# Optimization experiments

Hardware: AMD Instinct MI355X
Metric: run time of the kernel (lower is better)

## Reference

```python
import jax, jax.numpy as jnp
import numpy as np

B, F, H = 16384, 2048, 4096   # batch, n_features, n_hidden
D, K = 4096, 2048             # num_of_demos, num_of_features


def setup_inputs() -> dict:
    key = jax.random.key(0)
    ks = jax.random.split(key, 16)
    s = 0.02
    return {
        "x": jax.random.normal(ks[0], (B, F), jnp.float32),
        "demo_metric": jax.random.uniform(ks[1], (D, K), jnp.float32),
        "alpha": jax.random.normal(ks[2], (K,), jnp.float32),
        "sample_loss": jax.random.uniform(ks[3], (D, K), jnp.float32),
        "subdom_constant": jax.random.uniform(ks[4], (1,), jnp.float32),
        "num_of_demos": D,
        "num_of_features": K,
        "W1": jax.random.normal(ks[5], (F, H), jnp.float32) * s,
        "b1": jnp.zeros((H,), jnp.float32),
        "W2": jax.random.normal(ks[6], (H, H), jnp.float32) * s,
        "b2": jnp.zeros((H,), jnp.float32),
        "W3": jax.random.normal(ks[7], (H, H), jnp.float32) * s,
        "b3": jnp.zeros((H,), jnp.float32),
        "W4": jax.random.normal(ks[8], (H, 2), jnp.float32) * s,
        "b4": jnp.zeros((2,), jnp.float32),
    }


def reference(x, demo_metric, alpha, sample_loss, subdom_constant,
              num_of_demos, num_of_features,
              W1, b1, W2, b2, W3, b3, W4, b4):
    # subdom hinge loss: max(alpha_k * (sample_loss_jk - demo_loss_jk) + 1, 0) - c
    margin = alpha[None, :] * (sample_loss - demo_metric) + 1.0  # [D, K]
    subdom = jnp.maximum(margin, 0.0) - subdom_constant          # broadcast c
    loss = jnp.sum(subdom)

    # MLP classifier (dropout = identity at inference) + sigmoid
    h = jax.nn.relu(x @ W1 + b1)
    h = jax.nn.relu(h @ W2 + b2)
    h = jax.nn.relu(h @ W3 + b3)
    probs = jax.nn.sigmoid(h @ W4 + b4)  # [B, 2]
    return (loss, probs)
```

## Files before the change

### kernel.cpp

```cpp
#include <hip/hip_runtime.h>
#include <cstdint>
#include <cstddef>

typedef unsigned short u16;
typedef __attribute__((ext_vector_type(8))) __bf16 bf16x8;
typedef __attribute__((ext_vector_type(4))) float f32x4;

__device__ __forceinline__ u16 f2bf(float f) {
  union { float f; unsigned u; } v; v.f = f;
  unsigned r = v.u + 0x7FFFu + ((v.u >> 16) & 1u);
  return (u16)(r >> 16);
}
__device__ __forceinline__ float bf2f(unsigned h) {
  union { unsigned u; float f; } v; v.u = h << 16;
  return v.f;
}

__global__ void init_loss_kernel(const float* __restrict__ c,
                                 const int* __restrict__ D,
                                 const int* __restrict__ K,
                                 float* __restrict__ out) {
  out[0] = -c[0] * (float)D[0] * (float)K[0];
}

__global__ void subdom_kernel(const float4* __restrict__ dm,
                              const float4* __restrict__ sl,
                              const float4* __restrict__ alpha4,
                              float* __restrict__ out, int n4, int k4mask) {
  const int stride = gridDim.x * blockDim.x;
  float s = 0.f;
  for (int i = blockIdx.x * blockDim.x + threadIdx.x; i < n4; i += stride) {
    float4 d = dm[i], l = sl[i], a = alpha4[i & k4mask];
    s += fmaxf(fmaf(a.x, l.x - d.x, 1.f), 0.f);
    s += fmaxf(fmaf(a.y, l.y - d.y, 1.f), 0.f);
    s += fmaxf(fmaf(a.z, l.z - d.z, 1.f), 0.f);
    s += fmaxf(fmaf(a.w, l.w - d.w, 1.f), 0.f);
  }
#pragma unroll
  for (int off = 32; off > 0; off >>= 1) s += __shfl_down(s, off, 64);
  __shared__ float red[4];
  const int lane = threadIdx.x & 63, wave = threadIdx.x >> 6;
  if (lane == 0) red[wave] = s;
  __syncthreads();
  if (threadIdx.x == 0) atomicAdd(out, red[0] + red[1] + red[2] + red[3]);
}

__global__ void cast_f32_bf16_kernel(const float4* __restrict__ in,
                                     u16* __restrict__ out, int n4) {
  const int stride = gridDim.x * blockDim.x;
  for (int i = blockIdx.x * blockDim.x + threadIdx.x; i < n4; i += stride) {
    float4 v = in[i];
    uint2 p;
    p.x = (unsigned)f2bf(v.x) | ((unsigned)f2bf(v.y) << 16);
    p.y = (unsigned)f2bf(v.z) | ((unsigned)f2bf(v.w) << 16);
    ((uint2*)out)[i] = p;
  }
}

__global__ void transpose_cast_kernel(const float* __restrict__ in,
                                      u16* __restrict__ out, int K, int N) {
  __shared__ float tile[32][33];
  const int bx = blockIdx.x * 32;
  const int by = blockIdx.y * 32;
  const int tx = threadIdx.x, ty = threadIdx.y;
#pragma unroll
  for (int i = ty; i < 32; i += 8)
    tile[i][tx] = in[(size_t)(by + i) * N + bx + tx];
  __syncthreads();
#pragma unroll
  for (int i = ty; i < 32; i += 8)
    out[(size_t)(bx + i) * K + by + tx] = f2bf(tile[tx][i]);
}


__device__ __forceinline__ void gload_lds16(const void* g, void* l) {
  __builtin_amdgcn_global_load_lds(
      (const __attribute__((address_space(1))) void*)g,
      (__attribute__((address_space(3))) void*)l, 16, 0, 0);
}

#define VMW(N) asm volatile("s_waitcnt vmcnt(" #N ")" ::: "memory")
#define MF(a, b, c) __builtin_amdgcn_mfma_f32_16x16x32_bf16(a, b, c, 0, 0, 0)

#define STAGE_A(BU, Q, TK)                                                    \
  gload_lds16(A + aGbase + (size_t)((Q)*64) * K + (size_t)(TK)*64,            \
              (void*)(As + ((BU)*4 + (Q)) * 4096 + swave))

#define STAGE_B(BU, NH, HH, TK)                                               \
  gload_lds16(Bt + bGbase + (size_t)((NH)*32 + (HH)*128) * K +                \
                  (size_t)(TK)*64,                                            \
              (void*)(Bs + ((BU)*2 + (NH)) * 8192 + (HH)*4096 + swave))

#define BRD(BF, BU, NH2)                                                      \
  {                                                                           \
    const u16* Br_ = Bs + ((BU)*2 + (NH2)) * 8192 + bbase;                    \
    BF[0] = *(const bf16x8*)(Br_ + aslot0);                                   \
    BF[1] = *(const bf16x8*)(Br_ + aslot1);                                   \
    BF[2] = *(const bf16x8*)(Br_ + 1024 + aslot0);                            \
    BF[3] = *(const bf16x8*)(Br_ + 1024 + aslot1);                            \
  }

#define PH(BUF, MH, NH, LA, BF, PRE_CODE, STAGE_CODE, WAIT_CODE)              \
  {                                                                           \
    if (LA) {                                                                 \
      const u16* Ar_ = As + ((BUF)*4 + (wm << 1) + (MH)) * 4096 + abase;      \
      _Pragma("unroll") for (int f_ = 0; f_ < 4; ++f_) {                      \
        af0[f_] = *(const bf16x8*)(Ar_ + f_ * 1024 + aslot0);                 \
        af1[f_] = *(const bf16x8*)(Ar_ + f_ * 1024 + aslot1);                 \
      }                                                                       \
    }                                                                         \
    PRE_CODE;                                                                 \
    STAGE_CODE;                                                               \
    __builtin_amdgcn_s_setprio(1);                                            \
    _Pragma("unroll") for (int f_ = 0; f_ < 4; ++f_) {                        \
      acc[(MH)*4 + f_][(NH)*2 + 0] = MF(af0[f_], BF[0], acc[(MH)*4 + f_][(NH)*2 + 0]); \
      acc[(MH)*4 + f_][(NH)*2 + 0] = MF(af1[f_], BF[1], acc[(MH)*4 + f_][(NH)*2 + 0]); \
      acc[(MH)*4 + f_][(NH)*2 + 1] = MF(af0[f_], BF[2], acc[(MH)*4 + f_][(NH)*2 + 1]); \
      acc[(MH)*4 + f_][(NH)*2 + 1] = MF(af1[f_], BF[3], acc[(MH)*4 + f_][(NH)*2 + 1]); \
    }                                                                         \
    __builtin_amdgcn_s_setprio(0);                                            \
    WAIT_CODE;                                                                \
    __builtin_amdgcn_s_barrier();                                             \
  }

__global__ __launch_bounds__(512, 2) void gemm256(
    const u16* __restrict__ A, const u16* __restrict__ Bt,
    const float* __restrict__ bias, u16* __restrict__ C,
    int M, int N, int K, int act) {
  __shared__ __align__(16) u16 As[2 * 4 * 4096];
  __shared__ __align__(16) u16 Bs[2 * 2 * 8192];

  const int gx = gridDim.x;
  const int bid = blockIdx.x + blockIdx.y * gx;
  const int cpx = (gx * gridDim.y) >> 3;
  const int tilei = (bid & 7) * cpx + (bid >> 3);
  const int m0 = (tilei / gx) * 256;
  const int n0 = (tilei % gx) * 256;

  const int tid = threadIdx.x;
  const int wave = tid >> 6, lane = tid & 63;
  const int l15 = lane & 15, quad = lane >> 4;
  const int wm = wave >> 2, wn = wave & 3;
  const int lsw = l15 & 7;

  const int aslot0 = ((quad ^ lsw) << 3);
  const int aslot1 = (((4 + quad) ^ lsw) << 3);
  const int abase = l15 * 64;
  const int bbase = (wn * 32 + l15) * 64;

  const int srow = tid >> 3;
  const int skch = ((tid & 7) ^ (srow & 7)) << 3;
  const int brow = ((srow >> 5) << 6) + (srow & 31);
  const size_t aGbase = (size_t)(m0 + srow) * K + skch;
  const size_t bGbase = (size_t)(n0 + brow) * K + skch;
  const int swave = wave * 512;

  f32x4 acc[8][4];
#pragma unroll
  for (int i = 0; i < 8; ++i)
#pragma unroll
    for (int j = 0; j < 4; ++j) acc[i][j] = (f32x4){0.f, 0.f, 0.f, 0.f};
  bf16x8 af0[4], af1[4], bfr0[4], bfr1[4];

  STAGE_A(0, 0, 0); STAGE_A(0, 1, 0); STAGE_A(0, 2, 0); STAGE_A(0, 3, 0);
  STAGE_B(0, 0, 0, 0); STAGE_B(0, 0, 1, 0);
  STAGE_B(0, 1, 0, 0); STAGE_B(0, 1, 1, 0);
  STAGE_A(1, 0, 1); STAGE_A(1, 2, 1);
  VMW(2);
  __builtin_amdgcn_s_barrier();
  BRD(bfr0, 0, 0);

  const int niter = K >> 7;
  for (int it = 0; it < niter - 1; ++it) {
    const int t1 = 2 * it + 1, t2 = 2 * it + 2, t3 = 2 * it + 3;
    PH(0, 0, 0, 1, bfr0, {},
       { STAGE_B(1, 0, 0, t1); STAGE_B(1, 0, 1, t1); }, { VMW(6); });
    PH(0, 0, 1, 0, bfr1, BRD(bfr1, 0, 1),
       { STAGE_B(1, 1, 0, t1); STAGE_B(1, 1, 1, t1); }, { VMW(4); });
    PH(0, 1, 0, 1, bfr0, {},
       { STAGE_A(0, 0, t2); STAGE_A(0, 2, t2); }, { VMW(4); });
    PH(0, 1, 1, 0, bfr1, BRD(bfr0, 1, 0),
       { STAGE_A(1, 1, t1); STAGE_A(1, 3, t1); }, {});
    PH(1, 0, 0, 1, bfr0, {},
       { STAGE_B(0, 0, 0, t2); STAGE_B(0, 0, 1, t2); }, { VMW(6); });
    PH(1, 0, 1, 0, bfr1, BRD(bfr1, 1, 1),
       { STAGE_B(0, 1, 0, t2); STAGE_B(0, 1, 1, t2); }, { VMW(4); });
    PH(1, 1, 0, 1, bfr0, {},
       { STAGE_A(1, 0, t3); STAGE_A(1, 2, t3); }, { VMW(4); });
    PH(1, 1, 1, 0, bfr1, BRD(bfr0, 0, 0),
       { STAGE_A(0, 1, t2); STAGE_A(0, 3, t2); }, {});
  }
  {
    const int t1 = 2 * niter - 1;
    PH(0, 0, 0, 1, bfr0, {},
       { STAGE_B(1, 0, 0, t1); STAGE_B(1, 0, 1, t1); }, { VMW(6); });
    PH(0, 0, 1, 0, bfr1, BRD(bfr1, 0, 1),
       { STAGE_B(1, 1, 0, t1); STAGE_B(1, 1, 1, t1); }, { VMW(4); });
    PH(0, 1, 0, 1, bfr0, {}, {}, { VMW(2); });
    PH(0, 1, 1, 0, bfr1, BRD(bfr0, 1, 0),
       { STAGE_A(1, 1, t1); STAGE_A(1, 3, t1); }, {});
    PH(1, 0, 0, 1, bfr0, {}, {}, { VMW(2); });
    PH(1, 0, 1, 0, bfr1, BRD(bfr1, 1, 1), {}, { VMW(0); });
    PH(1, 1, 0, 1, bfr0, {}, {}, {});
    PH(1, 1, 1, 0, bfr1, {}, {}, {});
  }

#pragma unroll
  for (int mi = 0; mi < 8; ++mi) {
    const int row = m0 + wm * 128 + (mi >> 2) * 64 + (mi & 3) * 16 + quad * 4;
#pragma unroll
    for (int j = 0; j < 4; ++j) {
      const int col = n0 + wn * 64 + j * 16 + l15;
      const float bv = bias[col];
#pragma unroll
      for (int r = 0; r < 4; ++r) {
        float v = acc[mi][j][r] + bv;
        if (act) v = fmaxf(v, 0.f);
        C[(size_t)(row + r) * N + col] = f2bf(v);
      }
    }
  }
}

__global__ __launch_bounds__(256) void head_kernel(
    const u16* __restrict__ h, const float2* __restrict__ W4,
    const float* __restrict__ b4, float* __restrict__ out, int H) {
  const int row = blockIdx.x;
  const u16* hr = h + (size_t)row * H;
  const int tid = threadIdx.x;
  float p0 = 0.f, p1 = 0.f;
#pragma unroll
  for (int ii = 0; ii < 2; ++ii) {
    const int base = tid * 16 + ii * 8;
    const uint4 hv = *(const uint4*)(hr + base);
    const unsigned uu[4] = {hv.x, hv.y, hv.z, hv.w};
#pragma unroll
    for (int j = 0; j < 4; ++j) {
      float a0 = bf2f(uu[j] & 0xffffu);
      float a1 = bf2f(uu[j] >> 16);
      float2 w0 = W4[base + 2 * j];
      float2 w1 = W4[base + 2 * j + 1];
      p0 += a0 * w0.x + a1 * w1.x;
      p1 += a0 * w0.y + a1 * w1.y;
    }
  }
#pragma unroll
  for (int off = 32; off > 0; off >>= 1) {
    p0 += __shfl_down(p0, off, 64);
    p1 += __shfl_down(p1, off, 64);
  }
  __shared__ float r0[4], r1[4];
  const int lane = tid & 63, wave = tid >> 6;
  if (lane == 0) { r0[wave] = p0; r1[wave] = p1; }
  __syncthreads();
  if (tid == 0) {
    float l0 = r0[0] + r0[1] + r0[2] + r0[3] + b4[0];
    float l1 = r1[0] + r1[1] + r1[2] + r1[3] + b4[1];
    out[1 + row * 2] = 1.f / (1.f + __expf(-l0));
    out[2 + row * 2] = 1.f / (1.f + __expf(-l1));
  }
}

extern "C" void kernel_launch(void* const* d_in, const int* in_sizes, int n_in,
                              void* d_out, int out_size, void* d_ws,
                              size_t ws_size, hipStream_t stream) {
  (void)in_sizes; (void)n_in; (void)out_size; (void)ws_size;
  const float* x  = (const float*)d_in[0];
  const float* dm = (const float*)d_in[1];
  const float* al = (const float*)d_in[2];
  const float* sl = (const float*)d_in[3];
  const float* sc = (const float*)d_in[4];
  const int*   nd = (const int*)d_in[5];
  const int*   nf = (const int*)d_in[6];
  const float* W1 = (const float*)d_in[7];
  const float* b1 = (const float*)d_in[8];
  const float* W2 = (const float*)d_in[9];
  const float* b2 = (const float*)d_in[10];
  const float* W3 = (const float*)d_in[11];
  const float* b3 = (const float*)d_in[12];
  const float* W4 = (const float*)d_in[13];
  const float* b4 = (const float*)d_in[14];
  float* out = (float*)d_out;

  const int B = 16384, F = 2048, H = 4096, D = 4096, K = 2048;

  char* ws = (char*)d_ws;
  u16* xb = (u16*)ws;
  u16* wt = (u16*)(ws + (size_t)B * F * 2);
  u16* hA = (u16*)(ws + (size_t)B * F * 2 + (size_t)H * H * 2);
  u16* hB = hA + (size_t)B * H;

  init_loss_kernel<<<1, 1, 0, stream>>>(sc, nd, nf, out);
  subdom_kernel<<<1024, 256, 0, stream>>>((const float4*)dm, (const float4*)sl,
                                          (const float4*)al, out, D * K / 4,
                                          K / 4 - 1);
  cast_f32_bf16_kernel<<<4096, 256, 0, stream>>>((const float4*)x, xb, B * F / 4);
  transpose_cast_kernel<<<dim3(H / 32, F / 32), dim3(32, 8), 0, stream>>>(W1, wt, F, H);
  gemm256<<<dim3(H / 256, B / 256), 512, 0, stream>>>(xb, wt, b1, hA, B, H, F, 1);
  transpose_cast_kernel<<<dim3(H / 32, H / 32), dim3(32, 8), 0, stream>>>(W2, wt, H, H);
  gemm256<<<dim3(H / 256, B / 256), 512, 0, stream>>>(hA, wt, b2, hB, B, H, H, 1);
  transpose_cast_kernel<<<dim3(H / 32, H / 32), dim3(32, 8), 0, stream>>>(W3, wt, H, H);
  gemm256<<<dim3(H / 256, B / 256), 512, 0, stream>>>(hB, wt, b3, hA, B, H, H, 1);
  head_kernel<<<B, 256, 0, stream>>>(hA, (const float2*)W4, b4, out, H);
}
```

Before: 1.691 ms.

## Restructure GEMM pipeline to prefetch LDS fragments after MFMA and batch global stages

Reorders the software pipeline of the 256x256 bf16 GEMM so that LDS reads of A and B fragments for the next phase are issued after the current MFMA block, behind a sched_barrier, instead of before it. Global-to-LDS staging is regrouped into two larger batches per half-iteration, with the prologue staging only one K-tile. The goal is to hide LDS read latency behind MFMA work and to simplify the wait-count schedule. The risks are higher register pressure from holding prefetched fragments across barriers, and less overlap of global loads because the prologue stages less ahead.

Result: slower. 1.879 ms (+11.1%).

```diff
diff --git a/kernel.cpp b/kernel.cpp
--- a/kernel.cpp
+++ b/kernel.cpp
@@ -91,6 +91,15 @@
                   (size_t)(TK)*64,                                            \
               (void*)(Bs + ((BU)*2 + (NH)) * 8192 + (HH)*4096 + swave))
 
+#define ARD(BU, MH)                                                           \
+  {                                                                           \
+    const u16* Ar_ = As + ((BU)*4 + wm2 + (MH)) * 4096 + abase;               \
+    _Pragma("unroll") for (int f_ = 0; f_ < 4; ++f_) {                        \
+      af0[f_] = *(const bf16x8*)(Ar_ + f_ * 1024 + aslot0);                   \
+      af1[f_] = *(const bf16x8*)(Ar_ + f_ * 1024 + aslot1);                   \
+    }                                                                         \
+  }
+
 #define BRD(BF, BU, NH2)                                                      \
   {                                                                           \
     const u16* Br_ = Bs + ((BU)*2 + (NH2)) * 8192 + bbase;                    \
@@ -100,16 +109,8 @@
     BF[3] = *(const bf16x8*)(Br_ + 1024 + aslot1);                            \
   }
 
-#define PH(BUF, MH, NH, LA, BF, PRE_CODE, STAGE_CODE, WAIT_CODE)              \
+#define PH(MH, NH, BF, STAGE_CODE, POST_CODE, WAIT_CODE)                      \
   {                                                                           \
-    if (LA) {                                                                 \
-      const u16* Ar_ = As + ((BUF)*4 + (wm << 1) + (MH)) * 4096 + abase;      \
-      _Pragma("unroll") for (int f_ = 0; f_ < 4; ++f_) {                      \
-        af0[f_] = *(const bf16x8*)(Ar_ + f_ * 1024 + aslot0);                 \
-        af1[f_] = *(const bf16x8*)(Ar_ + f_ * 1024 + aslot1);                 \
-      }                                                                       \
-    }                                                                         \
-    PRE_CODE;                                                                 \
     STAGE_CODE;                                                               \
     __builtin_amdgcn_s_setprio(1);                                            \
     _Pragma("unroll") for (int f_ = 0; f_ < 4; ++f_) {                        \
@@ -119,6 +120,8 @@
       acc[(MH)*4 + f_][(NH)*2 + 1] = MF(af1[f_], BF[3], acc[(MH)*4 + f_][(NH)*2 + 1]); \
     }                                                                         \
     __builtin_amdgcn_s_setprio(0);                                            \
+    __builtin_amdgcn_sched_barrier(0);                                        \
+    POST_CODE;                                                                \
     WAIT_CODE;                                                                \
     __builtin_amdgcn_s_barrier();                                             \
   }
@@ -141,6 +144,7 @@
   const int wave = tid >> 6, lane = tid & 63;
   const int l15 = lane & 15, quad = lane >> 4;
   const int wm = wave >> 2, wn = wave & 3;
+  const int wm2 = wm << 1;
   const int lsw = l15 & 7;
 
   const int aslot0 = ((quad ^ lsw) << 3);
@@ -162,47 +166,55 @@
     for (int j = 0; j < 4; ++j) acc[i][j] = (f32x4){0.f, 0.f, 0.f, 0.f};
   bf16x8 af0[4], af1[4], bfr0[4], bfr1[4];
 
-  STAGE_A(0, 0, 0); STAGE_A(0, 1, 0); STAGE_A(0, 2, 0); STAGE_A(0, 3, 0);
+  STAGE_A(0, 0, 0); STAGE_A(0, 2, 0);
   STAGE_B(0, 0, 0, 0); STAGE_B(0, 0, 1, 0);
   STAGE_B(0, 1, 0, 0); STAGE_B(0, 1, 1, 0);
-  STAGE_A(1, 0, 1); STAGE_A(1, 2, 1);
+  STAGE_A(0, 1, 0); STAGE_A(0, 3, 0);
   VMW(2);
   __builtin_amdgcn_s_barrier();
+  ARD(0, 0);
   BRD(bfr0, 0, 0);
 
   const int niter = K >> 7;
   for (int it = 0; it < niter - 1; ++it) {
-    const int t1 = 2 * it + 1, t2 = 2 * it + 2, t3 = 2 * it + 3;
-    PH(0, 0, 0, 1, bfr0, {},
-       { STAGE_B(1, 0, 0, t1); STAGE_B(1, 0, 1, t1); }, { VMW(6); });
-    PH(0, 0, 1, 0, bfr1, BRD(bfr1, 0, 1),
-       { STAGE_B(1, 1, 0, t1); STAGE_B(1, 1, 1, t1); }, { VMW(4); });
-    PH(0, 1, 0, 1, bfr0, {},
-       { STAGE_A(0, 0, t2); STAGE_A(0, 2, t2); }, { VMW(4); });
-    PH(0, 1, 1, 0, bfr1, BRD(bfr0, 1, 0),
-       { STAGE_A(1, 1, t1); STAGE_A(1, 3, t1); }, {});
-    PH(1, 0, 0, 1, bfr0, {},
-       { STAGE_B(0, 0, 0, t2); STAGE_B(0, 0, 1, t2); }, { VMW(6); });
-    PH(1, 0, 1, 0, bfr1, BRD(bfr1, 1, 1),
-       { STAGE_B(0, 1, 0, t2); STAGE_B(0, 1, 1, t2); }, { VMW(4); });
-    PH(1, 1, 0, 1, bfr0, {},
-       { STAGE_A(1, 0, t3); STAGE_A(1, 2, t3); }, { VMW(4); });
-    PH(1, 1, 1, 0, bfr1, BRD(bfr0, 0, 0),
-       { STAGE_A(0, 1, t2); STAGE_A(0, 3, t2); }, {});
+    const int t1 = 2 * it + 1, t2 = 2 * it + 2;
+    PH(0, 0, bfr0,
+       { STAGE_A(1, 0, t1); STAGE_A(1, 2, t1);
+         STAGE_B(1, 0, 0, t1); STAGE_B(1, 0, 1, t1); },
+       { BRD(bfr1, 0, 1); }, { VMW(4); });
+    PH(0, 1, bfr1,
+       { STAGE_B(1, 1, 0, t1); STAGE_B(1, 1, 1, t1);
+         STAGE_A(1, 1, t1); STAGE_A(1, 3, t1); },
+       { ARD(0, 1); }, {});
+    PH(1, 0, bfr0, {}, {}, { VMW(4); });
+    PH(1, 1, bfr1, {}, { ARD(1, 0); BRD(bfr0, 1, 0); }, { VMW(2); });
+    PH(0, 0, bfr0,
+       { STAGE_A(0, 0, t2); STAGE_A(0, 2, t2);
+         STAGE_B(0, 0, 0, t2); STAGE_B(0, 0, 1, t2); },
+       { BRD(bfr1, 1, 1); }, { VMW(4); });
+    PH(0, 1, bfr1,
+       { STAGE_B(0, 1, 0, t2); STAGE_B(0, 1, 1, t2);
+         STAGE_A(0, 1, t2); STAGE_A(0, 3, t2); },
+       { ARD(1, 1); }, {});
+    PH(1, 0, bfr0, {}, {}, { VMW(4); });
+    PH(1, 1, bfr1, {}, { ARD(0, 0); BRD(bfr0, 0, 0); }, { VMW(2); });
   }
   {
     const int t1 = 2 * niter - 1;
-    PH(0, 0, 0, 1, bfr0, {},
-       { STAGE_B(1, 0, 0, t1); STAGE_B(1, 0, 1, t1); }, { VMW(6); });
-    PH(0, 0, 1, 0, bfr1, BRD(bfr1, 0, 1),
-       { STAGE_B(1, 1, 0, t1); STAGE_B(1, 1, 1, t1); }, { VMW(4); });
-    PH(0, 1, 0, 1, bfr0, {}, {}, { VMW(2); });
-    PH(0, 1, 1, 0, bfr1, BRD(bfr0, 1, 0),
-       { STAGE_A(1, 1, t1); STAGE_A(1, 3, t1); }, {});
-    PH(1, 0, 0, 1, bfr0, {}, {}, { VMW(2); });
-    PH(1, 0, 1, 0, bfr1, BRD(bfr1, 1, 1), {}, { VMW(0); });
-    PH(1, 1, 0, 1, bfr0, {}, {}, {});
-    PH(1, 1, 1, 0, bfr1, {}, {}, {});
+    PH(0, 0, bfr0,
+       { STAGE_A(1, 0, t1); STAGE_A(1, 2, t1);
+         STAGE_B(1, 0, 0, t1); STAGE_B(1, 0, 1, t1); },
+       { BRD(bfr1, 0, 1); }, { VMW(4); });
+    PH(0, 1, bfr1,
+       { STAGE_B(1, 1, 0, t1); STAGE_B(1, 1, 1, t1);
+         STAGE_A(1, 1, t1); STAGE_A(1, 3, t1); },
+       { ARD(0, 1); }, {});
+    PH(1, 0, bfr0, {}, {}, { VMW(4); });
+    PH(1, 1, bfr1, {}, { ARD(1, 0); BRD(bfr0, 1, 0); }, { VMW(2); });
+    PH(0, 0, bfr0, {}, { BRD(bfr1, 1, 1); }, { VMW(0); });
+    PH(0, 1, bfr1, {}, { ARD(1, 1); }, {});
+    PH(1, 0, bfr0, {}, {}, {});
+    PH(1, 1, bfr1, {}, {}, {});
   }
 
 #pragma unroll
```
